# Kernel tuning notes

Measured on AMD Instinct MI355X. Metric: run time of the kernel, lower is better.

Reference implementation:

```python
import jax, jax.numpy as jnp
import numpy as np

N_HEADS, N_KV, HEAD_DIM, D_MODEL, T_MAX = 16, 4, 64, 1024, 2048
GROUPS = N_HEADS // N_KV
EPS = 1e-6


def _rms_norm(x, w):
    # RMSNorm over last dim (head_dim), computed in fp32 like the torch module
    xf = x.astype(jnp.float32)
    r = jax.lax.rsqrt(jnp.mean(xf * xf, axis=-1, keepdims=True) + EPS)
    return (xf * r).astype(x.dtype) * w


def _apply_rope(x, cos, sin):
    # x: (B, H, T, D); cos/sin: (T_max, D/2)
    T = x.shape[2]
    c = cos[:T][None, None]  # (1,1,T,D/2)
    s = sin[:T][None, None]
    x1, x2 = jnp.split(x, 2, axis=-1)
    return jnp.concatenate([x1 * c - x2 * s, x2 * c + x1 * s], axis=-1)


def setup_inputs() -> dict:
    key = jax.random.key(0)
    ks = jax.random.split(key, 8)
    B, T = 2, 2048
    x = jax.random.normal(ks[0], (B, T, D_MODEL), dtype=jnp.float32)
    # realistic RoPE tables
    theta = 10000.0
    inv_freq = 1.0 / (theta ** (np.arange(0, HEAD_DIM, 2, dtype=np.float32) / HEAD_DIM))
    t = np.arange(T_MAX, dtype=np.float32)
    freqs = np.outer(t, inv_freq)  # (T_max, D/2)
    cos = jnp.asarray(np.cos(freqs))
    sin = jnp.asarray(np.sin(freqs))
    sd = 0.02
    wq = jax.random.normal(ks[1], (N_HEADS * HEAD_DIM, D_MODEL), dtype=jnp.float32) * sd
    wk = jax.random.normal(ks[2], (N_KV * HEAD_DIM, D_MODEL), dtype=jnp.float32) * sd
    wv = jax.random.normal(ks[3], (N_KV * HEAD_DIM, D_MODEL), dtype=jnp.float32) * sd
    wo = jax.random.normal(ks[4], (D_MODEL, N_HEADS * HEAD_DIM), dtype=jnp.float32) * sd
    qn_w = jnp.ones((HEAD_DIM,), dtype=jnp.float32)
    kn_w = jnp.ones((HEAD_DIM,), dtype=jnp.float32)
    return {"x": x, "cos": cos, "sin": sin, "wq": wq, "wk": wk, "wv": wv,
            "wo": wo, "qn_w": qn_w, "kn_w": kn_w}


def reference(x, cos, sin, wq, wk, wv, wo, qn_w, kn_w):
    B, T, _ = x.shape
    scale = HEAD_DIM ** -0.5
    # projections (torch Linear: y = x @ W.T)
    q = (x @ wq.T).reshape(B, T, N_HEADS, HEAD_DIM).transpose(0, 2, 1, 3)
    k = (x @ wk.T).reshape(B, T, N_KV, HEAD_DIM).transpose(0, 2, 1, 3)
    v = (x @ wv.T).reshape(B, T, N_KV, HEAD_DIM).transpose(0, 2, 1, 3)
    # qk RMSNorm
    q = _rms_norm(q, qn_w)
    k = _rms_norm(k, kn_w)
    # RoPE
    q = _apply_rope(q, cos, sin)
    k = _apply_rope(k, cos, sin)
    # GQA expansion: query head h uses kv head h // GROUPS
    k = jnp.repeat(k, GROUPS, axis=1)  # (B, H, T, D)
    v = jnp.repeat(v, GROUPS, axis=1)
    # causal SDPA
    scores = jnp.einsum('bhqd,bhkd->bhqk', q, k) * scale
    causal = jnp.tril(jnp.ones((T, T), dtype=bool))
    scores = jnp.where(causal, scores, jnp.finfo(scores.dtype).min)
    p = jax.nn.softmax(scores, axis=-1)
    out = jnp.einsum('bhqk,bhkd->bhqd', p, v)
    out = out.transpose(0, 2, 1, 3).reshape(B, T, N_HEADS * HEAD_DIM)
    return out @ wo.T
```

## Files before the change

kernel.cpp:

```cpp
#include <hip/hip_runtime.h>


typedef __bf16 bf16;
typedef __attribute__((ext_vector_type(8))) __bf16 bf16x8;
typedef __attribute__((ext_vector_type(4))) float f32x4;

#define MFMA(a, b, c) __builtin_amdgcn_mfma_f32_16x16x32_bf16((a), (b), (c), 0, 0, 0)
#define GLOAD_LDS16(g, l)                                        \
  __builtin_amdgcn_global_load_lds(                              \
      (const __attribute__((address_space(1))) void*)(g),        \
      (__attribute__((address_space(3))) void*)(l), 16, 0, 0)

__device__ __forceinline__ bool is_bf16_input(const void* cosRaw) {
  return ((const unsigned short*)cosRaw)[0] == 0x3F80;
}
__device__ __forceinline__ float rdval(const void* p, int idx, bool isbf) {
  return isbf ? (float)((const bf16*)p)[idx] : ((const float*)p)[idx];
}

__device__ __forceinline__ void stage_rows(const void* src, size_t rowbase,
                                           int ko, int srow, int csrc,
                                           int lane, bf16* ls, bool isbf) {
  if (isbf) {
    GLOAD_LDS16(&((const bf16*)src)[(rowbase + srow) * 1024 + ko + csrc * 8], ls);
  } else {
    const float* fp = &((const float*)src)[(rowbase + srow) * 1024 + ko + csrc * 8];
    float4 f0 = *(const float4*)fp;
    float4 f1 = *(const float4*)(fp + 4);
    bf16x8 o;
    o[0] = (bf16)f0.x; o[1] = (bf16)f0.y; o[2] = (bf16)f0.z; o[3] = (bf16)f0.w;
    o[4] = (bf16)f1.x; o[5] = (bf16)f1.y; o[6] = (bf16)f1.z; o[7] = (bf16)f1.w;
    *(bf16x8*)&ls[lane * 8] = o;
  }
}

__global__ __launch_bounds__(256, 6) void proj_kernel(
    const void* __restrict__ xraw, const void* __restrict__ wqraw,
    const void* __restrict__ wkraw, const void* __restrict__ wvraw,
    bf16* __restrict__ qp, bf16* __restrict__ kp, bf16* __restrict__ vt,
    const void* __restrict__ cosraw, const void* __restrict__ sinraw,
    const void* __restrict__ qnraw, const void* __restrict__ knraw) {
  __shared__ bf16 As[64 * 64];
  __shared__ bf16 Bs[64 * 64];

  const int idx = (int)blockIdx.x;
  const int xcd = idx & 7;
  const int jj = idx >> 3;
  const int mb = (jj & 7) * 8 + xcd;
  const int nb = jj >> 3;
  const int n0 = nb * 64;
  const int m0 = mb * 64;

  const int tid = threadIdx.x;
  const int wave = tid >> 6;
  const int lane = tid & 63;
  const int q16 = lane & 15;
  const int quad = lane >> 4;
  const int srow = lane >> 3;
  const int csrc = (lane & 7) ^ srow;
  const int wm = wave * 16;
  const int x7 = q16 & 7;
  const bool isbf = is_bf16_input(cosraw);

  const void* wsrc;
  int nr0;
  if (nb < 16)      { wsrc = wqraw; nr0 = n0; }
  else if (nb < 20) { wsrc = wkraw; nr0 = n0 - 1024; }
  else              { wsrc = wvraw; nr0 = n0 - 1280; }

  f32x4 acc[4];
#pragma unroll
  for (int nt = 0; nt < 4; ++nt) acc[nt] = (f32x4){0.f, 0.f, 0.f, 0.f};

  for (int kt = 0; kt < 16; ++kt) {
    const int ko = kt * 64;
#pragma unroll
    for (int i = 0; i < 2; ++i) {
      int rb = wave * 16 + i * 8;
      stage_rows(xraw, (size_t)(m0 + rb), ko, srow, csrc, lane, &As[rb * 64], isbf);
      stage_rows(wsrc, (size_t)(nr0 + rb), ko, srow, csrc, lane, &Bs[rb * 64], isbf);
    }
    __syncthreads();

    bf16x8 a0, a1, bfr[4][2];
    {
      const bf16* rp = &As[(wm + q16) * 64];
      a0 = *(const bf16x8*)&rp[(quad ^ x7) * 8];
      a1 = *(const bf16x8*)&rp[((quad + 4) ^ x7) * 8];
    }
#pragma unroll
    for (int nt = 0; nt < 4; ++nt) {
      const bf16* rp = &Bs[(nt * 16 + q16) * 64];
      bfr[nt][0] = *(const bf16x8*)&rp[(quad ^ x7) * 8];
      bfr[nt][1] = *(const bf16x8*)&rp[((quad + 4) ^ x7) * 8];
    }
#pragma unroll
    for (int nt = 0; nt < 4; ++nt) {
      acc[nt] = MFMA(a0, bfr[nt][0], acc[nt]);
      acc[nt] = MFMA(a1, bfr[nt][1], acc[nt]);
    }
    __syncthreads();
  }

  if (nb < 20) {
    const void* nwp = (nb < 16) ? qnraw : knraw;
    const float osc = (nb < 16) ? 0.125f : 1.0f;
    float wd[4];
#pragma unroll
    for (int nt = 0; nt < 4; ++nt) wd[nt] = rdval(nwp, nt * 16 + q16, isbf);

#pragma unroll
    for (int r = 0; r < 4; ++r) {
      float p = acc[0][r] * acc[0][r] + acc[1][r] * acc[1][r] +
                acc[2][r] * acc[2][r] + acc[3][r] * acc[3][r];
#pragma unroll
      for (int off = 8; off >= 1; off >>= 1) p += __shfl_xor(p, off);
      float rms = rsqrtf(p * (1.0f / 64.0f) + 1e-6f);

      int row = m0 + wm + quad * 4 + r;
      int t = row & 2047;
      float c0 = rdval(cosraw, t * 32 + q16, isbf);
      float c1 = rdval(cosraw, t * 32 + 16 + q16, isbf);
      float s0 = rdval(sinraw, t * 32 + q16, isbf);
      float s1 = rdval(sinraw, t * 32 + 16 + q16, isbf);

      float v0 = acc[0][r] * rms * wd[0];
      float v1 = acc[1][r] * rms * wd[1];
      float v2 = acc[2][r] * rms * wd[2];
      float v3 = acc[3][r] * rms * wd[3];

      bf16* op = (nb < 16) ? &qp[(size_t)row * 1024 + nb * 64]
                           : &kp[(size_t)row * 256 + (nb - 16) * 64];
      op[0 * 16 + q16] = (bf16)((v0 * c0 - v2 * s0) * osc);
      op[1 * 16 + q16] = (bf16)((v1 * c1 - v3 * s1) * osc);
      op[2 * 16 + q16] = (bf16)((v2 * c0 + v0 * s0) * osc);
      op[3 * 16 + q16] = (bf16)((v3 * c1 + v1 * s1) * osc);
    }
  } else {
    const int vh = nb - 20;
    const int b = m0 >> 11;
    const int tbase = m0 & 2047;
#pragma unroll
    for (int nt = 0; nt < 4; ++nt)
#pragma unroll
      for (int r = 0; r < 4; ++r)
        As[(wm + quad * 4 + r) * 64 + nt * 16 + q16] = (bf16)acc[nt][r];
    __syncthreads();
#pragma unroll
    for (int rep = 0; rep < 2; ++rep) {
      int c = tid + 256 * rep;
      int d = c >> 3;
      int t8 = (c & 7) * 8;
      bf16x8 pk;
#pragma unroll
      for (int j = 0; j < 8; ++j) pk[j] = As[(t8 + j) * 64 + d];
      *(bf16x8*)&vt[(((size_t)(b * 4 + vh)) * 64 + d) * 2048 + tbase + t8] = pk;
    }
  }
}

__global__ __launch_bounds__(256, 4) void flash_kernel(
    const bf16* __restrict__ qp, const bf16* __restrict__ kp,
    const bf16* __restrict__ vt, bf16* __restrict__ attn) {
  const int qblk = blockIdx.z ? 31 - (int)blockIdx.x : (int)blockIdx.x;
  const int h = blockIdx.y;
  const int b = blockIdx.z;
  const int kvh = h >> 2;
  const int tid = threadIdx.x;
  const int wave = tid >> 6;
  const int lane = tid & 63;
  const int q16 = lane & 15;
  const int quad = lane >> 4;
  const int r7 = q16 & 7;
  const int t0 = qblk * 64 + wave * 16;

  __shared__ bf16 Ks[2][64 * 64];
  __shared__ bf16 Vs[2][64 * 64];
  __shared__ bf16 Pl[4][16 * 32];

  const bf16* qrow = qp + (((size_t)(b * 2048 + t0 + q16)) * 16 + h) * 64;
  bf16x8 qa0 = *(const bf16x8*)(qrow + quad * 8);
  bf16x8 qa1 = *(const bf16x8*)(qrow + 32 + quad * 8);

  bf16x8 ones;
#pragma unroll
  for (int j = 0; j < 8; ++j) ones[j] = (bf16)1.0f;

  f32x4 O[4], l4;
#pragma unroll
  for (int nt = 0; nt < 4; ++nt) O[nt] = (f32x4){0.f, 0.f, 0.f, 0.f};
  l4 = (f32x4){0.f, 0.f, 0.f, 0.f};

  const int ntile = qblk + 1;

  bf16x8 kr[2], vr[2];
  const int cr = tid * 2;
  const int krow = cr >> 3;
  const size_t kgbase = (((size_t)(b * 2048) + krow) * 4 + kvh) * 64;
  const size_t vgbase = ((size_t)(b * 4 + kvh) * 64 + krow) * 2048;

  auto gload = [&](int tk) {
#pragma unroll
    for (int rep = 0; rep < 2; ++rep) {
      int ch = (cr + rep) & 7;
      kr[rep] = *(const bf16x8*)&kp[kgbase + (size_t)(tk * 64) * 256 + ch * 8];
      vr[rep] = *(const bf16x8*)&vt[vgbase + tk * 64 + ch * 8];
    }
  };
  auto swrite = [&](int bb) {
#pragma unroll
    for (int rep = 0; rep < 2; ++rep) {
      int ch = (cr + rep) & 7;
      int pos = (ch ^ (krow & 7)) * 8;
      *(bf16x8*)&Ks[bb][krow * 64 + pos] = kr[rep];
      *(bf16x8*)&Vs[bb][krow * 64 + pos] = vr[rep];
    }
  };

  gload(0);

  for (int t = 0; t < ntile; ++t) {
    const int bb = t & 1;
    const int kbase = t * 64;
    swrite(bb);
    __syncthreads();
    if (t + 1 < ntile) gload(t + 1);

    f32x4 s[4];
#pragma unroll
    for (int kt = 0; kt < 4; ++kt) {
      const bf16* kr0 = &Ks[bb][(kt * 16 + q16) * 64];
      bf16x8 kb0 = *(const bf16x8*)&kr0[(quad ^ r7) * 8];
      bf16x8 kb1 = *(const bf16x8*)&kr0[((quad + 4) ^ r7) * 8];
      f32x4 z = (f32x4){0.f, 0.f, 0.f, 0.f};
      z = MFMA(qa0, kb0, z);
      z = MFMA(qa1, kb1, z);
      s[kt] = z;
    }

    if (kbase + 63 > t0) {
#pragma unroll
      for (int kt = 0; kt < 4; ++kt) {
        int jt = kbase + kt * 16 + q16;
#pragma unroll
        for (int r = 0; r < 4; ++r)
          if (jt > t0 + quad * 4 + r) s[kt][r] = -1e30f;
      }
    }

#pragma unroll
    for (int kt = 0; kt < 4; ++kt)
#pragma unroll
      for (int r = 0; r < 4; ++r) s[kt][r] = __expf(s[kt][r] - 9.0f);

#pragma unroll
    for (int kh = 0; kh < 2; ++kh) {
#pragma unroll
      for (int ct = 0; ct < 2; ++ct) {
        const int kt = kh * 2 + ct;
#pragma unroll
        for (int r = 0; r < 4; ++r) {
          int row = quad * 4 + r;
          int col = ct * 16 + q16;
          Pl[wave][row * 32 + (((col >> 3) ^ (row & 3)) * 8) + (col & 7)] =
              (bf16)s[kt][r];
        }
      }
      bf16x8 pa = *(const bf16x8*)&Pl[wave][q16 * 32 + ((quad ^ (q16 & 3)) * 8)];
#pragma unroll
      for (int nt = 0; nt < 4; ++nt) {
        const bf16* vr0 = &Vs[bb][(nt * 16 + q16) * 64];
        bf16x8 vb = *(const bf16x8*)&vr0[((kh * 4 + quad) ^ r7) * 8];
        O[nt] = MFMA(pa, vb, O[nt]);
      }
      l4 = MFMA(pa, ones, l4);
    }
  }

  float inv[4];
#pragma unroll
  for (int r = 0; r < 4; ++r) inv[r] = 1.0f / l4[r];
#pragma unroll
  for (int nt = 0; nt < 4; ++nt)
#pragma unroll
    for (int r = 0; r < 4; ++r) {
      size_t o = (((size_t)(b * 2048 + t0 + quad * 4 + r)) * 16 + h) * 64 +
                 nt * 16 + q16;
      attn[o] = (bf16)(O[nt][r] * inv[r]);
    }
}

__global__ __launch_bounds__(256, 6) void gemm_o_kernel(
    const bf16* __restrict__ A, const void* __restrict__ Wraw,
    void* __restrict__ C, const void* __restrict__ cosraw) {
  __shared__ bf16 As[64 * 64];
  __shared__ bf16 Bs[64 * 64];

  const int idx = (int)blockIdx.x;
  const int xcd = idx & 7;
  const int jj = idx >> 3;
  const int mb = (jj & 7) * 8 + xcd;
  const int nb = jj >> 3;
  const int n0 = nb * 64;
  const int m0 = mb * 64;

  const int tid = threadIdx.x;
  const int wave = tid >> 6;
  const int lane = tid & 63;
  const int q16 = lane & 15;
  const int quad = lane >> 4;
  const int srow = lane >> 3;
  const int csrc = (lane & 7) ^ srow;
  const int wm = wave * 16;
  const int x7 = q16 & 7;
  const bool isbf = is_bf16_input(cosraw);

  f32x4 acc[4];
#pragma unroll
  for (int nt = 0; nt < 4; ++nt) acc[nt] = (f32x4){0.f, 0.f, 0.f, 0.f};

  for (int kt = 0; kt < 16; ++kt) {
    const int ko = kt * 64;
#pragma unroll
    for (int i = 0; i < 2; ++i) {
      int rb = wave * 16 + i * 8;
      GLOAD_LDS16(&A[(size_t)(m0 + rb + srow) * 1024 + ko + csrc * 8],
                  &As[rb * 64]);
      stage_rows(Wraw, (size_t)(n0 + rb), ko, srow, csrc, lane, &Bs[rb * 64], isbf);
    }
    __syncthreads();

    bf16x8 a0, a1, bfr[4][2];
    {
      const bf16* rp = &As[(wm + q16) * 64];
      a0 = *(const bf16x8*)&rp[(quad ^ x7) * 8];
      a1 = *(const bf16x8*)&rp[((quad + 4) ^ x7) * 8];
    }
#pragma unroll
    for (int nt = 0; nt < 4; ++nt) {
      const bf16* rp = &Bs[(nt * 16 + q16) * 64];
      bfr[nt][0] = *(const bf16x8*)&rp[(quad ^ x7) * 8];
      bfr[nt][1] = *(const bf16x8*)&rp[((quad + 4) ^ x7) * 8];
    }
#pragma unroll
    for (int nt = 0; nt < 4; ++nt) {
      acc[nt] = MFMA(a0, bfr[nt][0], acc[nt]);
      acc[nt] = MFMA(a1, bfr[nt][1], acc[nt]);
    }
    __syncthreads();
  }

#pragma unroll
  for (int nt = 0; nt < 4; ++nt)
#pragma unroll
    for (int r = 0; r < 4; ++r) {
      size_t idx2 = (size_t)(m0 + wm + quad * 4 + r) * 1024 + n0 + nt * 16 + q16;
      if (isbf) ((bf16*)C)[idx2] = (bf16)acc[nt][r];
      else      ((float*)C)[idx2] = acc[nt][r];
    }
}

extern "C" void kernel_launch(void* const* d_in, const int* in_sizes, int n_in,
                              void* d_out, int out_size, void* d_ws, size_t ws_size,
                              hipStream_t stream) {
  bf16* qp = (bf16*)d_ws;
  bf16* kp = qp + (size_t)4096 * 1024;
  bf16* vt = kp + (size_t)4096 * 256;
  bf16* at = vt + (size_t)4096 * 256;

  proj_kernel<<<1536, 256, 0, stream>>>(
      d_in[0], d_in[3], d_in[4], d_in[5], qp, kp, vt,
      d_in[1], d_in[2], d_in[7], d_in[8]);

  flash_kernel<<<dim3(32, 16, 2), 256, 0, stream>>>(qp, kp, vt, at);

  gemm_o_kernel<<<1024, 256, 0, stream>>>(at, d_in[6], d_out, d_in[1]);
}
```

Before: 173.4 us.

## Pre-convert inputs to bf16 and enlarge GEMM tiles to 128x64

Adds a conversion kernel that turns x and the Q/K/V weights into bf16 once, staging them in scratch space (the attention buffer and the output buffer). The projection GEMM can then use direct global-to-LDS loads instead of converting fp32 per tile. Both the projection and output GEMMs now use 128-row tiles with two M fragments per wave, which halves the block count and raises operand reuse. The cost is an extra kernel launch plus extra memory traffic, and lower occupancy from the larger tiles and launch-bound changes.

```diff
diff --git a/kernel.cpp b/kernel.cpp
--- a/kernel.cpp
+++ b/kernel.cpp
@@ -34,22 +34,50 @@
   }
 }
 
-__global__ __launch_bounds__(256, 6) void proj_kernel(
-    const void* __restrict__ xraw, const void* __restrict__ wqraw,
-    const void* __restrict__ wkraw, const void* __restrict__ wvraw,
+__global__ __launch_bounds__(256) void convert_kernel(
+    const void* __restrict__ x, const void* __restrict__ wq,
+    const void* __restrict__ wk, const void* __restrict__ wv,
+    bf16* __restrict__ dx, bf16* __restrict__ dw,
+    const void* __restrict__ cosraw) {
+  const bool isbf = is_bf16_input(cosraw);
+  const int c = (int)blockIdx.x * 256 + (int)threadIdx.x;
+  const void* src;
+  int off;
+  bf16* dst;
+  int dc;
+  if (c < 524288)      { src = x;  off = c;          dst = dx; dc = c; }
+  else if (c < 655360) { src = wq; off = c - 524288; dst = dw; dc = c - 524288; }
+  else if (c < 688128) { src = wk; off = c - 655360; dst = dw; dc = c - 524288; }
+  else                 { src = wv; off = c - 688128; dst = dw; dc = c - 524288; }
+  bf16x8 o;
+  if (isbf) {
+    o = ((const bf16x8*)src)[off];
+  } else {
+    const float4* fp = (const float4*)src + (size_t)off * 2;
+    float4 f0 = fp[0];
+    float4 f1 = fp[1];
+    o[0] = (bf16)f0.x; o[1] = (bf16)f0.y; o[2] = (bf16)f0.z; o[3] = (bf16)f0.w;
+    o[4] = (bf16)f1.x; o[5] = (bf16)f1.y; o[6] = (bf16)f1.z; o[7] = (bf16)f1.w;
+  }
+  ((bf16x8*)dst)[dc] = o;
+}
+
+__global__ __launch_bounds__(256, 3) void proj_kernel(
+    const bf16* __restrict__ xb, const bf16* __restrict__ wqb,
+    const bf16* __restrict__ wkb, const bf16* __restrict__ wvb,
     bf16* __restrict__ qp, bf16* __restrict__ kp, bf16* __restrict__ vt,
     const void* __restrict__ cosraw, const void* __restrict__ sinraw,
     const void* __restrict__ qnraw, const void* __restrict__ knraw) {
-  __shared__ bf16 As[64 * 64];
+  __shared__ bf16 As[128 * 64];
   __shared__ bf16 Bs[64 * 64];
 
   const int idx = (int)blockIdx.x;
   const int xcd = idx & 7;
   const int jj = idx >> 3;
-  const int mb = (jj & 7) * 8 + xcd;
-  const int nb = jj >> 3;
+  const int mb = (jj & 3) * 8 + xcd;
+  const int nb = jj >> 2;
   const int n0 = nb * 64;
-  const int m0 = mb * 64;
+  const int m0 = mb * 128;
 
   const int tid = threadIdx.x;
   const int wave = tid >> 6;
@@ -58,35 +86,42 @@
   const int quad = lane >> 4;
   const int srow = lane >> 3;
   const int csrc = (lane & 7) ^ srow;
-  const int wm = wave * 16;
   const int x7 = q16 & 7;
-  const bool isbf = is_bf16_input(cosraw);
-
-  const void* wsrc;
+
+  const bf16* wsrc;
   int nr0;
-  if (nb < 16)      { wsrc = wqraw; nr0 = n0; }
-  else if (nb < 20) { wsrc = wkraw; nr0 = n0 - 1024; }
-  else              { wsrc = wvraw; nr0 = n0 - 1280; }
-
-  f32x4 acc[4];
-#pragma unroll
-  for (int nt = 0; nt < 4; ++nt) acc[nt] = (f32x4){0.f, 0.f, 0.f, 0.f};
+  if (nb < 16)      { wsrc = wqb; nr0 = n0; }
+  else if (nb < 20) { wsrc = wkb; nr0 = n0 - 1024; }
+  else              { wsrc = wvb; nr0 = n0 - 1280; }
+
+  f32x4 acc[2][4];
+#pragma unroll
+  for (int mf = 0; mf < 2; ++mf)
+#pragma unroll
+    for (int nt = 0; nt < 4; ++nt) acc[mf][nt] = (f32x4){0.f, 0.f, 0.f, 0.f};
 
   for (int kt = 0; kt < 16; ++kt) {
     const int ko = kt * 64;
 #pragma unroll
+    for (int i = 0; i < 4; ++i) {
+      int rb = wave * 32 + i * 8;
+      GLOAD_LDS16(&xb[(size_t)(m0 + rb + srow) * 1024 + ko + csrc * 8],
+                  &As[rb * 64]);
+    }
+#pragma unroll
     for (int i = 0; i < 2; ++i) {
       int rb = wave * 16 + i * 8;
-      stage_rows(xraw, (size_t)(m0 + rb), ko, srow, csrc, lane, &As[rb * 64], isbf);
-      stage_rows(wsrc, (size_t)(nr0 + rb), ko, srow, csrc, lane, &Bs[rb * 64], isbf);
-    }
-    __syncthreads();
-
-    bf16x8 a0, a1, bfr[4][2];
-    {
-      const bf16* rp = &As[(wm + q16) * 64];
-      a0 = *(const bf16x8*)&rp[(quad ^ x7) * 8];
-      a1 = *(const bf16x8*)&rp[((quad + 4) ^ x7) * 8];
+      GLOAD_LDS16(&wsrc[(size_t)(nr0 + rb + srow) * 1024 + ko + csrc * 8],
+                  &Bs[rb * 64]);
+    }
+    __syncthreads();
+
+    bf16x8 a[2][2], bfr[4][2];
+#pragma unroll
+    for (int mf = 0; mf < 2; ++mf) {
+      const bf16* rp = &As[(wave * 32 + mf * 16 + q16) * 64];
+      a[mf][0] = *(const bf16x8*)&rp[(quad ^ x7) * 8];
+      a[mf][1] = *(const bf16x8*)&rp[((quad + 4) ^ x7) * 8];
     }
 #pragma unroll
     for (int nt = 0; nt < 4; ++nt) {
@@ -95,14 +130,17 @@
       bfr[nt][1] = *(const bf16x8*)&rp[((quad + 4) ^ x7) * 8];
     }
 #pragma unroll
-    for (int nt = 0; nt < 4; ++nt) {
-      acc[nt] = MFMA(a0, bfr[nt][0], acc[nt]);
-      acc[nt] = MFMA(a1, bfr[nt][1], acc[nt]);
-    }
+    for (int nt = 0; nt < 4; ++nt)
+#pragma unroll
+      for (int mf = 0; mf < 2; ++mf) {
+        acc[mf][nt] = MFMA(a[mf][0], bfr[nt][0], acc[mf][nt]);
+        acc[mf][nt] = MFMA(a[mf][1], bfr[nt][1], acc[mf][nt]);
+      }
     __syncthreads();
   }
 
   if (nb < 20) {
+    const bool isbf = is_bf16_input(cosraw);
     const void* nwp = (nb < 16) ? qnraw : knraw;
     const float osc = (nb < 16) ? 0.125f : 1.0f;
     float wd[4];
@@ -110,47 +148,53 @@
     for (int nt = 0; nt < 4; ++nt) wd[nt] = rdval(nwp, nt * 16 + q16, isbf);
 
 #pragma unroll
-    for (int r = 0; r < 4; ++r) {
-      float p = acc[0][r] * acc[0][r] + acc[1][r] * acc[1][r] +
-                acc[2][r] * acc[2][r] + acc[3][r] * acc[3][r];
-#pragma unroll
-      for (int off = 8; off >= 1; off >>= 1) p += __shfl_xor(p, off);
-      float rms = rsqrtf(p * (1.0f / 64.0f) + 1e-6f);
-
-      int row = m0 + wm + quad * 4 + r;
-      int t = row & 2047;
-      float c0 = rdval(cosraw, t * 32 + q16, isbf);
-      float c1 = rdval(cosraw, t * 32 + 16 + q16, isbf);
-      float s0 = rdval(sinraw, t * 32 + q16, isbf);
-      float s1 = rdval(sinraw, t * 32 + 16 + q16, isbf);
-
-      float v0 = acc[0][r] * rms * wd[0];
-      float v1 = acc[1][r] * rms * wd[1];
-      float v2 = acc[2][r] * rms * wd[2];
-      float v3 = acc[3][r] * rms * wd[3];
-
-      bf16* op = (nb < 16) ? &qp[(size_t)row * 1024 + nb * 64]
-                           : &kp[(size_t)row * 256 + (nb - 16) * 64];
-      op[0 * 16 + q16] = (bf16)((v0 * c0 - v2 * s0) * osc);
-      op[1 * 16 + q16] = (bf16)((v1 * c1 - v3 * s1) * osc);
-      op[2 * 16 + q16] = (bf16)((v2 * c0 + v0 * s0) * osc);
-      op[3 * 16 + q16] = (bf16)((v3 * c1 + v1 * s1) * osc);
+    for (int mf = 0; mf < 2; ++mf) {
+#pragma unroll
+      for (int r = 0; r < 4; ++r) {
+        float p = acc[mf][0][r] * acc[mf][0][r] + acc[mf][1][r] * acc[mf][1][r] +
+                  acc[mf][2][r] * acc[mf][2][r] + acc[mf][3][r] * acc[mf][3][r];
+#pragma unroll
+        for (int off = 8; off >= 1; off >>= 1) p += __shfl_xor(p, off);
+        float rms = rsqrtf(p * (1.0f / 64.0f) + 1e-6f);
+
+        int row = m0 + wave * 32 + mf * 16 + quad * 4 + r;
+        int t = row & 2047;
+        float c0 = rdval(cosraw, t * 32 + q16, isbf);
+        float c1 = rdval(cosraw, t * 32 + 16 + q16, isbf);
+        float s0 = rdval(sinraw, t * 32 + q16, isbf);
+        float s1 = rdval(sinraw, t * 32 + 16 + q16, isbf);
+
+        float v0 = acc[mf][0][r] * rms * wd[0];
+        float v1 = acc[mf][1][r] * rms * wd[1];
+        float v2 = acc[mf][2][r] * rms * wd[2];
+        float v3 = acc[mf][3][r] * rms * wd[3];
+
+        bf16* op = (nb < 16) ? &qp[(size_t)row * 1024 + nb * 64]
+                             : &kp[(size_t)row * 256 + (nb - 16) * 64];
+        op[0 * 16 + q16] = (bf16)((v0 * c0 - v2 * s0) * osc);
+        op[1 * 16 + q16] = (bf16)((v1 * c1 - v3 * s1) * osc);
+        op[2 * 16 + q16] = (bf16)((v2 * c0 + v0 * s0) * osc);
+        op[3 * 16 + q16] = (bf16)((v3 * c1 + v1 * s1) * osc);
+      }
     }
   } else {
     const int vh = nb - 20;
     const int b = m0 >> 11;
     const int tbase = m0 & 2047;
 #pragma unroll
-    for (int nt = 0; nt < 4; ++nt)
-#pragma unroll
-      for (int r = 0; r < 4; ++r)
-        As[(wm + quad * 4 + r) * 64 + nt * 16 + q16] = (bf16)acc[nt][r];
-    __syncthreads();
-#pragma unroll
-    for (int rep = 0; rep < 2; ++rep) {
+    for (int mf = 0; mf < 2; ++mf)
+#pragma unroll
+      for (int nt = 0; nt < 4; ++nt)
+#pragma unroll
+        for (int r = 0; r < 4; ++r)
+          As[(wave * 32 + mf * 16 + quad * 4 + r) * 64 + nt * 16 + q16] =
+              (bf16)acc[mf][nt][r];
+    __syncthreads();
+#pragma unroll
+    for (int rep = 0; rep < 4; ++rep) {
       int c = tid + 256 * rep;
-      int d = c >> 3;
-      int t8 = (c & 7) * 8;
+      int d = c >> 4;
+      int t8 = (c & 15) * 8;
       bf16x8 pk;
 #pragma unroll
       for (int j = 0; j < 8; ++j) pk[j] = As[(t8 + j) * 64 + d];
@@ -290,19 +334,19 @@
     }
 }
 
-__global__ __launch_bounds__(256, 6) void gemm_o_kernel(
+__global__ __launch_bounds__(256, 2) void gemm_o_kernel(
     const bf16* __restrict__ A, const void* __restrict__ Wraw,
     void* __restrict__ C, const void* __restrict__ cosraw) {
-  __shared__ bf16 As[64 * 64];
+  __shared__ bf16 As[128 * 64];
   __shared__ bf16 Bs[64 * 64];
 
   const int idx = (int)blockIdx.x;
   const int xcd = idx & 7;
   const int jj = idx >> 3;
-  const int mb = (jj & 7) * 8 + xcd;
-  const int nb = jj >> 3;
+  const int mb = (jj & 3) * 8 + xcd;
+  const int nb = jj >> 2;
   const int n0 = nb * 64;
-  const int m0 = mb * 64;
+  const int m0 = mb * 128;
 
   const int tid = threadIdx.x;
   const int wave = tid >> 6;
@@ -311,30 +355,36 @@
   const int quad = lane >> 4;
   const int srow = lane >> 3;
   const int csrc = (lane & 7) ^ srow;
-  const int wm = wave * 16;
   const int x7 = q16 & 7;
   const bool isbf = is_bf16_input(cosraw);
 
-  f32x4 acc[4];
-#pragma unroll
-  for (int nt = 0; nt < 4; ++nt) acc[nt] = (f32x4){0.f, 0.f, 0.f, 0.f};
+  f32x4 acc[2][4];
+#pragma unroll
+  for (int mf = 0; mf < 2; ++mf)
+#pragma unroll
+    for (int nt = 0; nt < 4; ++nt) acc[mf][nt] = (f32x4){0.f, 0.f, 0.f, 0.f};
 
   for (int kt = 0; kt < 16; ++kt) {
     const int ko = kt * 64;
 #pragma unroll
+    for (int i = 0; i < 4; ++i) {
+      int rb = wave * 32 + i * 8;
+      GLOAD_LDS16(&A[(size_t)(m0 + rb + srow) * 1024 + ko + csrc * 8],
+                  &As[rb * 64]);
+    }
+#pragma unroll
     for (int i = 0; i < 2; ++i) {
       int rb = wave * 16 + i * 8;
-      GLOAD_LDS16(&A[(size_t)(m0 + rb + srow) * 1024 + ko + csrc * 8],
-                  &As[rb * 64]);
       stage_rows(Wraw, (size_t)(n0 + rb), ko, srow, csrc, lane, &Bs[rb * 64], isbf);
     }
     __syncthreads();
 
-    bf16x8 a0, a1, bfr[4][2];
-    {
-      const bf16* rp = &As[(wm + q16) * 64];
-      a0 = *(const bf16x8*)&rp[(quad ^ x7) * 8];
-      a1 = *(const bf16x8*)&rp[((quad + 4) ^ x7) * 8];
+    bf16x8 a[2][2], bfr[4][2];
+#pragma unroll
+    for (int mf = 0; mf < 2; ++mf) {
+      const bf16* rp = &As[(wave * 32 + mf * 16 + q16) * 64];
+      a[mf][0] = *(const bf16x8*)&rp[(quad ^ x7) * 8];
+      a[mf][1] = *(const bf16x8*)&rp[((quad + 4) ^ x7) * 8];
     }
 #pragma unroll
     for (int nt = 0; nt < 4; ++nt) {
@@ -343,21 +393,26 @@
       bfr[nt][1] = *(const bf16x8*)&rp[((quad + 4) ^ x7) * 8];
     }
 #pragma unroll
-    for (int nt = 0; nt < 4; ++nt) {
-      acc[nt] = MFMA(a0, bfr[nt][0], acc[nt]);
-      acc[nt] = MFMA(a1, bfr[nt][1], acc[nt]);
-    }
-    __syncthreads();
-  }
-
-#pragma unroll
-  for (int nt = 0; nt < 4; ++nt)
-#pragma unroll
-    for (int r = 0; r < 4; ++r) {
-      size_t idx2 = (size_t)(m0 + wm + quad * 4 + r) * 1024 + n0 + nt * 16 + q16;
-      if (isbf) ((bf16*)C)[idx2] = (bf16)acc[nt][r];
-      else      ((float*)C)[idx2] = acc[nt][r];
-    }
+    for (int nt = 0; nt < 4; ++nt)
+#pragma unroll
+      for (int mf = 0; mf < 2; ++mf) {
+        acc[mf][nt] = MFMA(a[mf][0], bfr[nt][0], acc[mf][nt]);
+        acc[mf][nt] = MFMA(a[mf][1], bfr[nt][1], acc[mf][nt]);
+      }
+    __syncthreads();
+  }
+
+#pragma unroll
+  for (int mf = 0; mf < 2; ++mf)
+#pragma unroll
+    for (int nt = 0; nt < 4; ++nt)
+#pragma unroll
+      for (int r = 0; r < 4; ++r) {
+        size_t idx2 = (size_t)(m0 + wave * 32 + mf * 16 + quad * 4 + r) * 1024 +
+                      n0 + nt * 16 + q16;
+        if (isbf) ((bf16*)C)[idx2] = (bf16)acc[mf][nt][r];
+        else      ((float*)C)[idx2] = acc[mf][nt][r];
+      }
 }
 
 extern "C" void kernel_launch(void* const* d_in, const int* in_sizes, int n_in,
@@ -368,11 +423,19 @@
   bf16* vt = kp + (size_t)4096 * 256;
   bf16* at = vt + (size_t)4096 * 256;
 
-  proj_kernel<<<1536, 256, 0, stream>>>(
-      d_in[0], d_in[3], d_in[4], d_in[5], qp, kp, vt,
+  bf16* xb = at;
+  bf16* wqb = (bf16*)d_out;
+  bf16* wkb = wqb + (size_t)1048576;
+  bf16* wvb = wkb + (size_t)262144;
+
+  convert_kernel<<<2816, 256, 0, stream>>>(
+      d_in[0], d_in[3], d_in[4], d_in[5], xb, wqb, d_in[1]);
+
+  proj_kernel<<<768, 256, 0, stream>>>(
+      xb, wqb, wkb, wvb, qp, kp, vt,
       d_in[1], d_in[2], d_in[7], d_in[8]);
 
   flash_kernel<<<dim3(32, 16, 2), 256, 0, stream>>>(qp, kp, vt, at);
 
-  gemm_o_kernel<<<1024, 256, 0, stream>>>(at, d_in[6], d_out, d_in[1]);
-}
+  gemm_o_kernel<<<512, 256, 0, stream>>>(at, d_in[6], d_out, d_in[1]);
+}
```

Result: faster. 165.8 us (-4.4%).
